# Optimization experiments

Hardware: AMD Instinct MI355X
Metric: run time of the kernel (lower is better)

The kernel has to match this reference:

```python
import jax, jax.numpy as jnp
import numpy as np

B, S, E = 4, 1024, 1280
H = 16
D = E // H  # 80


def rotate_half(x):
    x1, x2 = jnp.split(x, 2, axis=-1)
    return jnp.concatenate([-x2, x1], axis=-1)


def setup_inputs() -> dict:
    key = jax.random.key(0)
    ks = jax.random.split(key, 12)
    sc = 0.02
    x = jax.random.normal(ks[0], (B, S, E), dtype=jnp.float32)
    # variable per-item sequence lengths (each <= S), cumulative
    lens = np.array([1024, 896, 768, 640], dtype=np.int32)
    cu_seqlens = jnp.asarray(np.concatenate([[0], np.cumsum(lens)]), dtype=jnp.int32)
    # rotary cos/sin for positions 0..S-1, head_dim D
    inv_freq = 1.0 / (10000.0 ** (np.arange(0, D, 2, dtype=np.float32) / D))
    t = np.arange(S, dtype=np.float32)
    freqs = np.outer(t, inv_freq)               # [S, D/2]
    emb = np.concatenate([freqs, freqs], axis=-1)  # [S, D]
    cos = jnp.asarray(np.cos(emb), dtype=jnp.float32)
    sin = jnp.asarray(np.sin(emb), dtype=jnp.float32)
    wq = jax.random.normal(ks[1], (E, E), dtype=jnp.float32) * sc
    bq = jax.random.normal(ks[2], (E,), dtype=jnp.float32) * sc
    wk = jax.random.normal(ks[3], (E, E), dtype=jnp.float32) * sc
    bk = jax.random.normal(ks[4], (E,), dtype=jnp.float32) * sc
    wv = jax.random.normal(ks[5], (E, E), dtype=jnp.float32) * sc
    bv = jax.random.normal(ks[6], (E,), dtype=jnp.float32) * sc
    wo = jax.random.normal(ks[7], (E, E), dtype=jnp.float32) * sc
    bo = jax.random.normal(ks[8], (E,), dtype=jnp.float32) * sc
    return {"x": x, "cu_seqlens": cu_seqlens, "cos": cos, "sin": sin,
            "wq": wq, "bq": bq, "wk": wk, "bk": bk, "wv": wv, "bv": bv,
            "wo": wo, "bo": bo}


def reference(x, cu_seqlens, cos, sin, wq, bq, wk, bk, wv, bv, wo, bo):
    b, s, e = x.shape
    h, d = H, D
    # QKV projections (nn.Linear: x @ W^T + b)
    q = (x @ wq.T + bq).reshape(b, s, h, d)
    k = (x @ wk.T + bk).reshape(b, s, h, d)
    v = (x @ wv.T + bv).reshape(b, s, h, d)
    # rotary embedding (apply_rotary_pos_emb, 'normal')
    c = cos[None, :, None, :]  # [1, s, 1, d]
    sn = sin[None, :, None, :]
    q = q * c + rotate_half(q) * sn
    k = k * c + rotate_half(k) * sn
    # patch attention mask from cu_seqlens (flatten_batch=False):
    # token i attends to token j iff i < len_b and j < len_b
    seq_lens = cu_seqlens[1:] - cu_seqlens[:-1]          # [b]
    idx = jnp.arange(s)
    valid = idx[None, :] < seq_lens[:, None]             # [b, s]
    mask = valid[:, None, :, None] & valid[:, None, None, :]  # [b, 1, s, s]
    # SDPA, non-causal
    scale = 1.0 / jnp.sqrt(jnp.asarray(d, dtype=q.dtype))
    scores = jnp.einsum("bqhd,bkhd->bhqk", q, k) * scale
    scores = jnp.where(mask, scores, jnp.asarray(-1e9, dtype=scores.dtype))
    attn = jax.nn.softmax(scores, axis=-1)
    out = jnp.einsum("bhqk,bkhd->bqhd", attn, v)         # [b, s, h, d]
    out = out.reshape(b, s, e)
    # output projection
    return out @ wo.T + bo
```

## Files before the change

### kernel.cpp

```cpp
#include <hip/hip_runtime.h>
#include <hip/hip_bf16.h>

#define B_ 4
#define S_ 1024
#define E_ 1280
#define H_ 16
#define D_ 80
#define M_ (B_*S_)

typedef __hip_bfloat16 bf16;
using bf16x8 = __attribute__((ext_vector_type(8))) short;
using f32x4  = __attribute__((ext_vector_type(4))) float;

__device__ __forceinline__ float b2f(bf16 x){ return __bfloat162float(x); }
__device__ __forceinline__ bf16  f2b(float x){ return __float2bfloat16(x); }
__device__ __forceinline__ void  stf(float* p, float v){ *p = v; }
__device__ __forceinline__ void  stf(bf16*  p, float v){ *p = f2b(v); }

__device__ __forceinline__ void gload_lds16(const void* g, void* l) {
    __builtin_amdgcn_global_load_lds(
        (const __attribute__((address_space(1))) unsigned int*)g,
        (__attribute__((address_space(3))) unsigned int*)l, 16, 0, 0);
}

__global__ __launch_bounds__(256) void cvt_kernel(
    const float* __restrict__ s0, const float* __restrict__ s1,
    const float* __restrict__ s2, const float* __restrict__ s3,
    const float* __restrict__ s4,
    bf16* __restrict__ d0, bf16* __restrict__ d1, bf16* __restrict__ d2,
    bf16* __restrict__ d3, bf16* __restrict__ d4,
    int n0, int n1)
{
    const float* s; bf16* d; int n;
    switch (blockIdx.y) {
        case 0: s = s0; d = d0; n = n0; break;
        case 1: s = s1; d = d1; n = n1; break;
        case 2: s = s2; d = d2; n = n1; break;
        case 3: s = s3; d = d3; n = n1; break;
        default: s = s4; d = d4; n = n1; break;
    }
    int i = (blockIdx.x * 256 + threadIdx.x) * 8;
    if (i >= n) return;
    float4 a = *(const float4*)(s + i);
    float4 b = *(const float4*)(s + i + 4);
    bf16 t[8];
    t[0]=f2b(a.x); t[1]=f2b(a.y); t[2]=f2b(a.z); t[3]=f2b(a.w);
    t[4]=f2b(b.x); t[5]=f2b(b.y); t[6]=f2b(b.z); t[7]=f2b(b.w);
    *(uint4*)(d + i) = *(const uint4*)t;
}

template<typename TC, bool VT_OUT>
__global__ __launch_bounds__(256) void mfma_gemm_bt(
    const bf16* __restrict__ A,
    const bf16* __restrict__ W0, const bf16* __restrict__ W1, const bf16* __restrict__ W2,
    const float* __restrict__ b0, const float* __restrict__ b1, const float* __restrict__ b2,
    TC* __restrict__ C0, TC* __restrict__ C1, TC* __restrict__ C2,
    int K, int N, int ntiles)
{
    const int mat = blockIdx.y / ntiles;
    const int bn  = (blockIdx.y % ntiles) * 128;
    const int bm  = blockIdx.x * 128;
    const bf16* W; const float* bias; TC* C;
    if (mat == 0)      { W = W0; bias = b0; C = C0; }
    else if (mat == 1) { W = W1; bias = b1; C = C1; }
    else               { W = W2; bias = b2; C = C2; }

    __shared__ bf16 As[2][128][32];
    __shared__ bf16 Ws[2][128][32];

    const int tid  = threadIdx.x;
    const int lane = tid & 63;
    const int wv   = tid >> 6;
    const int wm   = (wv & 1) * 64;
    const int wn   = (wv >> 1) * 64;
    const int srow = wv * 16 + (lane >> 2);
    const int scol = (lane & 3) * 8;

    f32x4 acc[4][4] = {};

    for (int k0 = 0; k0 < K; k0 += 64) {
        __syncthreads();
        #pragma unroll
        for (int p = 0; p < 2; p++) {
            const int kc = k0 + p*32 + scol;
            gload_lds16(A + (size_t)(bm + srow)      * K + kc, &As[p][wv*16][0]);
            gload_lds16(A + (size_t)(bm + 64 + srow) * K + kc, &As[p][64 + wv*16][0]);
            gload_lds16(W + (size_t)(bn + srow)      * K + kc, &Ws[p][wv*16][0]);
            gload_lds16(W + (size_t)(bn + 64 + srow) * K + kc, &Ws[p][64 + wv*16][0]);
        }
        __syncthreads();

        const int fr = lane & 15;
        const int kq = (lane >> 4) * 8;
        #pragma unroll
        for (int p = 0; p < 2; p++) {
            bf16x8 af[4], wf[4];
            #pragma unroll
            for (int t = 0; t < 4; t++) {
                af[t] = *(const bf16x8*)&As[p][wm + t*16 + fr][kq];
                wf[t] = *(const bf16x8*)&Ws[p][wn + t*16 + fr][kq];
            }
            #pragma unroll
            for (int mt = 0; mt < 4; mt++)
                #pragma unroll
                for (int nt = 0; nt < 4; nt++)
                    acc[mt][nt] = __builtin_amdgcn_mfma_f32_16x16x32_bf16(
                        af[mt], wf[nt], acc[mt][nt], 0, 0, 0);
        }
    }

    const int col_l = lane & 15;
    const int row_l = (lane >> 4) * 4;

    if (VT_OUT && mat == 2) {
        const int btok = bm >> 10;
        const int keyb = (bm & 1023) + wm + row_l;
        #pragma unroll
        for (int nt = 0; nt < 4; nt++) {
            const int n = bn + wn + nt*16 + col_l;
            const float bv = bias[n];
            const int hh = n / 80, dd = n % 80;
            bf16* vbase = (bf16*)C + ((size_t)(btok*H_ + hh)*D_ + dd)*S_ + keyb;
            #pragma unroll
            for (int mt = 0; mt < 4; mt++) {
                union { bf16 h[4]; uint2 u; } t4;
                #pragma unroll
                for (int r = 0; r < 4; r++) t4.h[r] = f2b(acc[mt][nt][r] + bv);
                *(uint2*)&vbase[mt*16] = t4.u;
            }
        }
    } else {
        #pragma unroll
        for (int nt = 0; nt < 4; nt++) {
            const int n = bn + wn + nt*16 + col_l;
            const float bv = bias[n];
            #pragma unroll
            for (int mt = 0; mt < 4; mt++) {
                #pragma unroll
                for (int r = 0; r < 4; r++) {
                    const int m = bm + wm + mt*16 + row_l + r;
                    stf(&C[(size_t)m * N + n], acc[mt][nt][r] + bv);
                }
            }
        }
    }
}

__device__ __forceinline__ void rope8(const bf16* lo, const bf16* hi,
                                      const float* cp, const float* sp,
                                      float mul, uint4* out_lo, uint4* out_hi)
{
    union { uint4 u; bf16 h[8]; } li, hi_, lo_o, hi_o;
    li.u  = *(const uint4*)lo;
    hi_.u = *(const uint4*)hi;
    #pragma unroll
    for (int u = 0; u < 8; u++) {
        float x1 = b2f(li.h[u]), x2 = b2f(hi_.h[u]);
        float c = cp[u], s = sp[u];
        lo_o.h[u] = f2b((x1*c - x2*s) * mul);
        hi_o.h[u] = f2b((x2*c + x1*s) * mul);
    }
    *out_lo = lo_o.u;
    *out_hi = hi_o.u;
}

__global__ __launch_bounds__(256, 4) void attn_mfma(
    const bf16* __restrict__ q, const bf16* __restrict__ k, const bf16* __restrict__ vt,
    const int* __restrict__ cu, const float* __restrict__ cosp, const float* __restrict__ sinp,
    bf16* __restrict__ o)
{
    __shared__ __align__(16) char smem[38144];
    bf16* Qs  = (bf16*)smem;
    bf16* Ks  = (bf16*)(smem + 13312);
    bf16* VTs = (bf16*)(smem + 26624);

    const int L  = blockIdx.x;
    const int qt = L >> 6;
    const int g  = L & 63;
    const int b  = g >> 4;
    const int h  = g & 15;

    const int tid = threadIdx.x;
    const int lane = tid & 63, wv = tid >> 6;
    const int quad = lane >> 4, l15 = lane & 15;
    const int q0 = qt * 64;
    const int len = cu[b + 1] - cu[b];
    const float scale = 0.11180339887498949f;

    #pragma unroll
    for (int i = 0; i < 2; i++) {
        int c = tid + i * 256;
        if (c < 320) {
            int row = c / 5, pc = c % 5;
            int s = q0 + row;
            const bf16* src = q + (size_t)(b*S_ + s)*E_ + h*D_ + pc*8;
            uint4 olo, ohi;
            rope8(src, src + 40, cosp + s*D_ + pc*8, sinp + s*D_ + pc*8, scale, &olo, &ohi);
            *(uint4*)&Qs[row*104 + pc*8]      = olo;
            *(uint4*)&Qs[row*104 + (pc+5)*8]  = ohi;
        }
    }
    if (tid < 128) {
        uint4 z = make_uint4(0,0,0,0);
        int row = tid >> 1, c8 = 10 + (tid & 1);
        *(uint4*)&Qs[row*104 + c8*8] = z;
        *(uint4*)&Ks[row*104 + c8*8] = z;
    }
    __syncthreads();

    bf16x8 qf[3];
    #pragma unroll
    for (int ks = 0; ks < 3; ks++)
        qf[ks] = *(const bf16x8*)&Qs[(wv*16 + l15)*104 + ks*32 + quad*8];

    float m_r[4], l_r[4];
    #pragma unroll
    for (int r = 0; r < 4; r++) { m_r[r] = -1e30f; l_r[r] = 0.f; }
    f32x4 o_acc[5] = {};
    bf16* PT = (bf16*)(smem + wv * 2304);

    const bool q_full = (q0 + 64) <= len;

    for (int kt = 0; kt < 16; kt++) {
        __syncthreads();
        #pragma unroll
        for (int i = 0; i < 2; i++) {
            int c = tid + i * 256;
            if (c < 320) {
                int row = c / 5, pc = c % 5;
                int s = kt*64 + row;
                const bf16* src = k + (size_t)(b*S_ + s)*E_ + h*D_ + pc*8;
                uint4 olo, ohi;
                rope8(src, src + 40, cosp + s*D_ + pc*8, sinp + s*D_ + pc*8, 1.0f, &olo, &ohi);
                *(uint4*)&Ks[row*104 + pc*8]      = olo;
                *(uint4*)&Ks[row*104 + (pc+5)*8]  = ohi;
            }
        }
        #pragma unroll
        for (int i = 0; i < 3; i++) {
            int c = tid + i * 256;
            if (c < 640) {
                int d = c >> 3, kc = c & 7;
                *(uint4*)&VTs[d*72 + kc*8] =
                    *(const uint4*)(vt + ((size_t)(b*H_ + h)*D_ + d)*S_ + kt*64 + kc*8);
            }
        }
        __syncthreads();

        f32x4 s4[4];
        #pragma unroll
        for (int nt = 0; nt < 4; nt++) {
            f32x4 a0 = {};
            #pragma unroll
            for (int ks = 0; ks < 3; ks++) {
                bf16x8 kf = *(const bf16x8*)&Ks[(nt*16 + l15)*104 + ks*32 + quad*8];
                a0 = __builtin_amdgcn_mfma_f32_16x16x32_bf16(qf[ks], kf, a0, 0, 0, 0);
            }
            s4[nt] = a0;
        }

        const bool full = q_full && (kt*64 + 64) <= len;

        float sv[4][4];
        if (full) {
            #pragma unroll
            for (int r = 0; r < 4; r++)
                #pragma unroll
                for (int nt = 0; nt < 4; nt++)
                    sv[nt][r] = s4[nt][r];
        } else {
            bool vk[4];
            #pragma unroll
            for (int nt = 0; nt < 4; nt++) vk[nt] = (kt*64 + nt*16 + l15) < len;
            #pragma unroll
            for (int r = 0; r < 4; r++) {
                const bool vq = (q0 + wv*16 + quad*4 + r) < len;
                #pragma unroll
                for (int nt = 0; nt < 4; nt++)
                    sv[nt][r] = (vq && vk[nt]) ? s4[nt][r] : -1e9f;
            }
        }
        float rmax[4];
        #pragma unroll
        for (int r = 0; r < 4; r++)
            rmax[r] = fmaxf(fmaxf(sv[0][r], sv[1][r]), fmaxf(sv[2][r], sv[3][r]));
        #pragma unroll
        for (int st = 1; st < 16; st <<= 1)
            #pragma unroll
            for (int r = 0; r < 4; r++)
                rmax[r] = fmaxf(rmax[r], __shfl_xor(rmax[r], st, 64));
        float mnew[4], alpha[4], rsum[4], p[4][4];
        #pragma unroll
        for (int r = 0; r < 4; r++) {
            mnew[r]  = fmaxf(m_r[r], rmax[r]);
            alpha[r] = __expf(m_r[r] - mnew[r]);
            float a = 0.f;
            #pragma unroll
            for (int nt = 0; nt < 4; nt++) { p[nt][r] = __expf(sv[nt][r] - mnew[r]); a += p[nt][r]; }
            rsum[r] = a;
        }
        #pragma unroll
        for (int st = 1; st < 16; st <<= 1)
            #pragma unroll
            for (int r = 0; r < 4; r++)
                rsum[r] += __shfl_xor(rsum[r], st, 64);
        #pragma unroll
        for (int r = 0; r < 4; r++) {
            l_r[r] = l_r[r] * alpha[r] + rsum[r];
            m_r[r] = mnew[r];
        }
        #pragma unroll
        for (int dt = 0; dt < 5; dt++)
            #pragma unroll
            for (int r = 0; r < 4; r++)
                o_acc[dt][r] *= alpha[r];
        #pragma unroll
        for (int nt = 0; nt < 4; nt++)
            #pragma unroll
            for (int r = 0; r < 4; r++)
                PT[(quad*4 + r)*72 + nt*16 + l15] = f2b(p[nt][r]);

        bf16x8 pa[2];
        #pragma unroll
        for (int ks = 0; ks < 2; ks++)
            pa[ks] = *(const bf16x8*)&PT[l15*72 + ks*32 + quad*8];
        #pragma unroll
        for (int dt = 0; dt < 5; dt++) {
            #pragma unroll
            for (int ks = 0; ks < 2; ks++) {
                bf16x8 vf = *(const bf16x8*)&VTs[(dt*16 + l15)*72 + ks*32 + quad*8];
                o_acc[dt] = __builtin_amdgcn_mfma_f32_16x16x32_bf16(pa[ks], vf, o_acc[dt], 0, 0, 0);
            }
        }
    }

    #pragma unroll
    for (int r = 0; r < 4; r++) {
        const float inv = 1.0f / l_r[r];
        size_t row_g = (size_t)(b*S_ + q0 + wv*16 + quad*4 + r);
        #pragma unroll
        for (int dt = 0; dt < 5; dt++)
            o[row_g*E_ + h*D_ + dt*16 + l15] = f2b(o_acc[dt][r] * inv);
    }
}

extern "C" void kernel_launch(void* const* d_in, const int* in_sizes, int n_in,
                              void* d_out, int out_size, void* d_ws, size_t ws_size,
                              hipStream_t stream)
{
    const float* x    = (const float*)d_in[0];
    const int*   cu   = (const int*)  d_in[1];
    const float* cosp = (const float*)d_in[2];
    const float* sinp = (const float*)d_in[3];
    const float* wq   = (const float*)d_in[4];
    const float* bq   = (const float*)d_in[5];
    const float* wk   = (const float*)d_in[6];
    const float* bk   = (const float*)d_in[7];
    const float* wv   = (const float*)d_in[8];
    const float* bv   = (const float*)d_in[9];
    const float* wo   = (const float*)d_in[10];
    const float* bo   = (const float*)d_in[11];
    float* out = (float*)d_out;

    bf16* q   = (bf16*)d_ws;
    bf16* kk  = q   + (size_t)M_ * E_;
    bf16* vt  = kk  + (size_t)M_ * E_;
    bf16* ao  = vt  + (size_t)M_ * E_;
    bf16* xb  = ao  + (size_t)M_ * E_;
    bf16* wqb = xb  + (size_t)M_ * E_;
    bf16* wkb = wqb + (size_t)E_ * E_;
    bf16* wvb = wkb + (size_t)E_ * E_;
    bf16* wob = wvb + (size_t)E_ * E_;

    cvt_kernel<<<dim3(2560, 5), 256, 0, stream>>>(
        x, wq, wk, wv, wo, xb, wqb, wkb, wvb, wob, M_*E_, E_*E_);

    mfma_gemm_bt<bf16, true><<<dim3(M_/128, 30), 256, 0, stream>>>(
        xb, wqb, wkb, wvb, bq, bk, bv, q, kk, vt, E_, E_, 10);

    attn_mfma<<<1024, 256, 0, stream>>>(q, kk, vt, cu, cosp, sinp, ao);

    mfma_gemm_bt<float, false><<<dim3(M_/128, 10), 256, 0, stream>>>(
        ao, wob, wob, wob, bo, bo, bo, out, out, out, E_, E_, 10);
}
```

Measured before the change: 274.3 us.

## Skip padded rows in Q/K projection and attention using sequence lengths

The Q and K projection GEMM now returns early for 128-row tiles that lie entirely past the sequence length. V is still computed in full. A new kernel computes the per-head mean of V over all positions, and attention tiles whose queries are all padding write that mean directly, matching the reference's uniform softmax over -1e9 masked scores. When the length is a multiple of 64, attention also loops only over valid key tiles and skips masking. This cuts GEMM and attention work for the padded tokens at the cost of an extra small kernel launch.

```diff
diff --git a/kernel.cpp b/kernel.cpp
--- a/kernel.cpp
+++ b/kernel.cpp
@@ -49,12 +49,13 @@
     *(uint4*)(d + i) = *(const uint4*)t;
 }
 
-template<typename TC, bool VT_OUT>
+template<typename TC, bool VT_OUT, bool SKIP_DEAD>
 __global__ __launch_bounds__(256) void mfma_gemm_bt(
     const bf16* __restrict__ A,
     const bf16* __restrict__ W0, const bf16* __restrict__ W1, const bf16* __restrict__ W2,
     const float* __restrict__ b0, const float* __restrict__ b1, const float* __restrict__ b2,
     TC* __restrict__ C0, TC* __restrict__ C1, TC* __restrict__ C2,
+    const int* __restrict__ cu,
     int K, int N, int ntiles)
 {
     const int mat = blockIdx.y / ntiles;
@@ -65,6 +66,12 @@
     else if (mat == 1) { W = W1; bias = b1; C = C1; }
     else               { W = W2; bias = b2; C = C2; }
 
+    if (SKIP_DEAD && mat < 2) {
+        const int bb = bm >> 10;
+        const int len = cu[bb + 1] - cu[bb];
+        if ((bm & 1023) >= len) return;
+    }
+
     __shared__ bf16 As[2][128][32];
     __shared__ bf16 Ws[2][128][32];
 
@@ -143,6 +150,32 @@
                 }
             }
         }
+    }
+}
+
+__global__ __launch_bounds__(256) void vsum_kernel(
+    const bf16* __restrict__ vt, float* __restrict__ vs)
+{
+    const int bh = blockIdx.x;
+    const bf16* base = vt + (size_t)bh * D_ * S_;
+    __shared__ float part[320];
+    for (int t = threadIdx.x; t < 320; t += 256) {
+        int d = t >> 2, qq = t & 3;
+        const bf16* p = base + (size_t)d * S_ + qq * 256;
+        float s = 0.f;
+        for (int i = 0; i < 32; i++) {
+            union { uint4 u; bf16 h[8]; } c;
+            c.u = *(const uint4*)(p + i*8);
+            #pragma unroll
+            for (int u = 0; u < 8; u++) s += b2f(c.h[u]);
+        }
+        part[t] = s;
+    }
+    __syncthreads();
+    if (threadIdx.x < 80) {
+        int d = threadIdx.x;
+        vs[(size_t)bh * D_ + d] =
+            (part[d*4] + part[d*4+1] + part[d*4+2] + part[d*4+3]) * (1.0f / 1024.0f);
     }
 }
 
@@ -167,7 +200,7 @@
 __global__ __launch_bounds__(256, 4) void attn_mfma(
     const bf16* __restrict__ q, const bf16* __restrict__ k, const bf16* __restrict__ vt,
     const int* __restrict__ cu, const float* __restrict__ cosp, const float* __restrict__ sinp,
-    bf16* __restrict__ o)
+    const float* __restrict__ vs, bf16* __restrict__ o)
 {
     __shared__ __align__(16) char smem[38144];
     bf16* Qs  = (bf16*)smem;
@@ -186,6 +219,27 @@
     const int q0 = qt * 64;
     const int len = cu[b + 1] - cu[b];
     const float scale = 0.11180339887498949f;
+
+    if (q0 >= len) {
+        const float* vsp = vs + (size_t)(b*H_ + h)*D_;
+        float v5[5];
+        #pragma unroll
+        for (int dt = 0; dt < 5; dt++) v5[dt] = vsp[dt*16 + l15];
+        #pragma unroll
+        for (int r = 0; r < 4; r++) {
+            size_t row_g = (size_t)(b*S_ + q0 + wv*16 + quad*4 + r);
+            #pragma unroll
+            for (int dt = 0; dt < 5; dt++)
+                o[row_g*E_ + h*D_ + dt*16 + l15] = f2b(v5[dt]);
+        }
+        return;
+    }
+
+    const bool cleanlen = ((len & 63) == 0);
+    const int  ktiles   = cleanlen ? (len >> 6) : 16;
+    const bool domask   = !cleanlen;
+
+    bf16* PT = (bf16*)(smem + wv * 2304);
 
     #pragma unroll
     for (int i = 0; i < 2; i++) {
@@ -207,7 +261,6 @@
         *(uint4*)&Ks[row*104 + c8*8] = z;
     }
     __syncthreads();
-
     bf16x8 qf[3];
     #pragma unroll
     for (int ks = 0; ks < 3; ks++)
@@ -217,11 +270,10 @@
     #pragma unroll
     for (int r = 0; r < 4; r++) { m_r[r] = -1e30f; l_r[r] = 0.f; }
     f32x4 o_acc[5] = {};
-    bf16* PT = (bf16*)(smem + wv * 2304);
 
     const bool q_full = (q0 + 64) <= len;
 
-    for (int kt = 0; kt < 16; kt++) {
+    for (int kt = 0; kt < ktiles; kt++) {
         __syncthreads();
         #pragma unroll
         for (int i = 0; i < 2; i++) {
@@ -259,10 +311,8 @@
             s4[nt] = a0;
         }
 
-        const bool full = q_full && (kt*64 + 64) <= len;
-
         float sv[4][4];
-        if (full) {
+        if (!domask || (q_full && (kt*64 + 64) <= len)) {
             #pragma unroll
             for (int r = 0; r < 4; r++)
                 #pragma unroll
@@ -371,15 +421,18 @@
     bf16* wkb = wqb + (size_t)E_ * E_;
     bf16* wvb = wkb + (size_t)E_ * E_;
     bf16* wob = wvb + (size_t)E_ * E_;
+    float* vsum = (float*)(wob + (size_t)E_ * E_);
 
     cvt_kernel<<<dim3(2560, 5), 256, 0, stream>>>(
         x, wq, wk, wv, wo, xb, wqb, wkb, wvb, wob, M_*E_, E_*E_);
 
-    mfma_gemm_bt<bf16, true><<<dim3(M_/128, 30), 256, 0, stream>>>(
-        xb, wqb, wkb, wvb, bq, bk, bv, q, kk, vt, E_, E_, 10);
-
-    attn_mfma<<<1024, 256, 0, stream>>>(q, kk, vt, cu, cosp, sinp, ao);
-
-    mfma_gemm_bt<float, false><<<dim3(M_/128, 10), 256, 0, stream>>>(
-        ao, wob, wob, wob, bo, bo, bo, out, out, out, E_, E_, 10);
-}
+    mfma_gemm_bt<bf16, true, true><<<dim3(M_/128, 30), 256, 0, stream>>>(
+        xb, wqb, wkb, wvb, bq, bk, bv, q, kk, vt, cu, E_, E_, 10);
+
+    vsum_kernel<<<64, 256, 0, stream>>>(vt, vsum);
+
+    attn_mfma<<<1024, 256, 0, stream>>>(q, kk, vt, cu, cosp, sinp, vsum, ao);
+
+    mfma_gemm_bt<float, false, false><<<dim3(M_/128, 10), 256, 0, stream>>>(
+        ao, wob, wob, wob, bo, bo, bo, out, out, out, cu, E_, E_, 10);
+}
```

Result: slower. 282.3 us (+2.9%).
